# Optimization experiments

Hardware: AMD Instinct MI355X
Metric: run time of the kernel (lower is better)

## Reference

```python
import jax, jax.numpy as jnp
import numpy as np

B, S, D, H = 2, 2048, 2048, 16
DH = D // H  # 128


def _rope(x, cos, sin):
    # Faithful to the source: x is (B, H, S, Dh) (already transposed), and the
    # original apply_rotary_emb slices freqs_cis[:, :H, :] and broadcasts over
    # the S axis -> rotation angle depends on head index (source quirk).
    h = x.shape[1]
    c = cos[:, :h, :][:, :, None, :]  # (1, H, 1, Dh/2)
    s = sin[:, :h, :][:, :, None, :]
    half = x.shape[-1] // 2
    re, im = x[..., :half], x[..., half:]
    return jnp.concatenate([re * c - im * s, re * s + im * c], axis=-1)


def setup_inputs() -> dict:
    key = jax.random.key(0)
    k0, k1, k2 = jax.random.split(key, 3)
    x = jax.random.normal(k0, (B, S, D), jnp.float32)
    Wqkv = jax.random.normal(k1, (D, 3 * D), jnp.float32) / np.float32(np.sqrt(D))
    bqkv = jnp.zeros((3 * D,), jnp.float32)
    Wout = jax.random.normal(k2, (D, D), jnp.float32) / np.float32(np.sqrt(D))
    bout = jnp.zeros((D,), jnp.float32)
    # standard RoPE frequency table, stored as cos/sin (unit-modulus complex)
    inv_freq = 1.0 / (10000.0 ** (np.arange(0, DH // 2, dtype=np.float32) / (DH // 2)))
    ang = np.outer(np.arange(S, dtype=np.float32), inv_freq)  # (S, Dh/2)
    freqs_cos = jnp.asarray(np.cos(ang)[None], jnp.float32)   # (1, S, Dh/2)
    freqs_sin = jnp.asarray(np.sin(ang)[None], jnp.float32)
    mask = jnp.triu(jnp.ones((S, S), bool), 1)[None, None]    # causal, True = masked
    return {"x": x, "Wqkv": Wqkv, "bqkv": bqkv, "Wout": Wout, "bout": bout,
            "freqs_cos": freqs_cos, "freqs_sin": freqs_sin, "mask": mask}


def reference(x, Wqkv, bqkv, Wout, bout, freqs_cos, freqs_sin, mask):
    b, s, d = x.shape
    scale = DH ** (-0.5)
    qkv = x @ Wqkv + bqkv                                   # (B, S, 3D)
    q, k, v = jnp.split(qkv, 3, axis=-1)
    to_heads = lambda t: t.reshape(b, s, H, DH).transpose(0, 2, 1, 3)  # (B,H,S,Dh)
    q, k, v = to_heads(q), to_heads(k), to_heads(v)
    q = _rope(q, freqs_cos, freqs_sin)
    k = _rope(k, freqs_cos, freqs_sin)
    scores = jnp.einsum('bhqd,bhkd->bhqk', q, k) * scale
    scores = jnp.where(mask, -jnp.inf, scores)
    p = jax.nn.softmax(scores, axis=-1)                     # dropout p=0 (eval)
    out = jnp.einsum('bhqk,bhkd->bhqd', p, v)
    out = out.transpose(0, 2, 1, 3).reshape(b, s, d)
    return out @ Wout + bout
```

## Files before the change

kernel.cpp:

```cpp
#include <hip/hip_runtime.h>

#define S_ 2048
#define D_ 2048
#define H_ 16
#define DH_ 128

typedef __attribute__((ext_vector_type(8))) short short8;
typedef __attribute__((ext_vector_type(4))) float f32x4;
typedef __attribute__((ext_vector_type(8))) unsigned short ushort8;
typedef __attribute__((ext_vector_type(4))) unsigned short ushort4v;

__device__ __forceinline__ unsigned short f2bf(float f) {
  unsigned int u;
  __builtin_memcpy(&u, &f, 4);
  unsigned int lsb = (u >> 16) & 1u;
  u += 0x7fffu + lsb;
  return (unsigned short)(u >> 16);
}

__device__ __forceinline__ void gload_lds16(const void* g, void* l) {
  __builtin_amdgcn_global_load_lds(
      (const __attribute__((address_space(1))) unsigned int*)g,
      (__attribute__((address_space(3))) unsigned int*)l, 16, 0, 0);
}

template <int N> __device__ __forceinline__ void vmwait() {
  if constexpr (N == 8)      asm volatile("s_waitcnt vmcnt(8)" ::: "memory");
  else if constexpr (N == 6) asm volatile("s_waitcnt vmcnt(6)" ::: "memory");
  else if constexpr (N == 4) asm volatile("s_waitcnt vmcnt(4)" ::: "memory");
  else if constexpr (N == 3) asm volatile("s_waitcnt vmcnt(3)" ::: "memory");
  else if constexpr (N == 2) asm volatile("s_waitcnt vmcnt(2)" ::: "memory");
  else                       asm volatile("s_waitcnt vmcnt(0)" ::: "memory");
}

#define FENCE_ asm volatile("" ::: "memory")
#define BAR_ { FENCE_; __builtin_amdgcn_s_barrier(); FENCE_; }

__global__ void k_convert_x(const float* __restrict__ x, unsigned short* __restrict__ xb) {
  int idx = blockIdx.x * 256 + threadIdx.x;
  const float4* xv = (const float4*)x;
  float4 a = xv[(size_t)idx * 2];
  float4 b = xv[(size_t)idx * 2 + 1];
  ushort8 o;
  o[0] = f2bf(a.x); o[1] = f2bf(a.y); o[2] = f2bf(a.z); o[3] = f2bf(a.w);
  o[4] = f2bf(b.x); o[5] = f2bf(b.y); o[6] = f2bf(b.z); o[7] = f2bf(b.w);
  *(ushort8*)(xb + (size_t)idx * 8) = o;
}

__global__ void k_prep_w(const float* __restrict__ W, const float* __restrict__ cosb,
                         const float* __restrict__ sinb, unsigned short* __restrict__ WT,
                         int Nw, int rot_limit) {
  __shared__ float tile[32][129];
  const int t = threadIdx.x;
  const int kt = blockIdx.x * 32, nt = blockIdx.y * 128;
#pragma unroll
  for (int i = 0; i < 4; ++i) {
    int q = i * 256 + t;
    int kl = q >> 5, cq = q & 31;
    float4 v = *(const float4*)(W + (size_t)(kt + kl) * Nw + nt + cq * 4);
    tile[kl][cq * 4 + 0] = v.x; tile[kl][cq * 4 + 1] = v.y;
    tile[kl][cq * 4 + 2] = v.z; tile[kl][cq * 4 + 3] = v.w;
  }
  __syncthreads();
  const bool rot = nt < rot_limit;
#pragma unroll
  for (int i = 0; i < 16; ++i) {
    int f = i * 256 + t;
    int kl = f & 31, nl = f >> 5;
    int ng = nt + nl;
    float val;
    if (rot) {
      int i0 = nl & 63;
      int h = (ng & 2047) >> 7;
      float c = cosb[h * 64 + i0], sn = sinb[h * 64 + i0];
      float re = tile[kl][i0], im = tile[kl][i0 + 64];
      val = (nl < 64) ? (re * c - im * sn) : (re * sn + im * c);
    } else {
      val = tile[kl][nl];
    }
    WT[(size_t)ng * 2048 + kt + kl] = f2bf(val);
  }
}

template <int NF, int MODE>
__global__ __launch_bounds__(512, 2) void k_ms(
    const unsigned short* __restrict__ A, const unsigned short* __restrict__ Bt,
    const float* __restrict__ bias,
    unsigned short* __restrict__ Qb, unsigned short* __restrict__ Kb,
    unsigned short* __restrict__ Vt, float* __restrict__ Co) {
  constexpr int BN = NF * 64;
  constexpr int NT = 32;
  constexpr int BBASE = 65536;
  constexpr int BSZ = BN * 128;
  __shared__ unsigned char lds[BBASE + 3 * BSZ];

  const int tid = threadIdx.x, l = tid & 63, w = tid >> 6;
  const int wm = w >> 2, wn = w & 3;
  const int nwg = gridDim.x;
  const int bid = blockIdx.x;
  const int swz = (bid & 7) * (nwg >> 3) + (bid >> 3);
  const int tm = (swz & 15) * 256;
  const int tn = (swz >> 4) * BN;

  const int sslot = (l & 7) ^ (l >> 3);
  const unsigned short* aB = A + (size_t)(tm + (l >> 3)) * 2048 + sslot * 8;
  const unsigned short* bB = Bt + (size_t)(tn + (l >> 3)) * 2048 + sslot * 8;
  const int xg = ((l >> 4) ^ (l & 7)) << 4;
  const int afo = (wm * 128 + (l & 15)) * 128 + xg;
  const int bfo = (wn * (NF * 16) + (l & 15)) * 128 + xg;

  f32x4 acc[8][NF] = {};
  short8 af[8], bf[2 * NF];

#define SAF_(ab_, u_) {                                                         \
  _Pragma("unroll") for (int i_ = 0; i_ < 4; ++i_) {                            \
    int c_ = w + i_ * 8;                                                        \
    gload_lds16(aB + (size_t)(c_ * 8) * 2048 + (u_) * 64,                       \
                lds + (ab_) + c_ * 1024); } }
#define SBF_(bs_, u_) {                                                         \
  _Pragma("unroll") for (int i_ = 0; i_ < NF; ++i_) {                           \
    int c_ = w + i_ * 8;                                                        \
    gload_lds16(bB + (size_t)(c_ * 8) * 2048 + (u_) * 64,                       \
                lds + (bs_) + c_ * 1024); } }
#define RDA2_(ab_, mh_) {                                                       \
  _Pragma("unroll") for (int m_ = 0; m_ < 4; ++m_) {                            \
    unsigned a_ = (ab_) + afo + ((mh_) * 4 + m_) * 2048;                        \
    af[m_]     = *(const short8*)(lds + a_);                                    \
    af[4 + m_] = *(const short8*)(lds + (a_ ^ 64)); } }
#define RDB2_(bb_) {                                                            \
  _Pragma("unroll") for (int n_ = 0; n_ < NF; ++n_) {                           \
    unsigned a_ = (bb_) + bfo + n_ * 2048;                                      \
    bf[n_]      = *(const short8*)(lds + a_);                                   \
    bf[NF + n_] = *(const short8*)(lds + (a_ ^ 64)); } }
#define MMF_(mh_) { __builtin_amdgcn_s_setprio(1);                              \
  _Pragma("unroll") for (int kk_ = 0; kk_ < 2; ++kk_)                           \
  _Pragma("unroll") for (int m_ = 0; m_ < 4; ++m_)                              \
  _Pragma("unroll") for (int n_ = 0; n_ < NF; ++n_)                             \
    acc[(mh_) * 4 + m_][n_] = __builtin_amdgcn_mfma_f32_16x16x32_bf16(          \
        af[kk_ * 4 + m_], bf[kk_ * NF + n_], acc[(mh_) * 4 + m_][n_], 0, 0, 0); \
  __builtin_amdgcn_s_setprio(0); }

  SAF_(0u, 0); SBF_(BBASE, 0); SBF_(BBASE + BSZ, 1);
  vmwait<NF>(); BAR_;

  int bcur = 0, bstg = 2;
#pragma unroll 1
  for (int v = 0; v < NT; ++v) {
    const unsigned ab = (unsigned)(v & 1) * 32768u;
    const unsigned an = (unsigned)((v + 1) & 1) * 32768u;
    const unsigned bb = BBASE + (unsigned)bcur * BSZ;
    const unsigned bs = BBASE + (unsigned)bstg * BSZ;
    RDB2_(bb);
    RDA2_(ab, 0);
    if (v + 1 < NT) SAF_(an, v + 1);
    MMF_(0);
    RDA2_(ab, 1);
    if (v + 2 < NT) SBF_(bs, v + 2);
    MMF_(1);
    if (v < NT - 2) { vmwait<NF>(); } else { vmwait<0>(); }
    BAR_;
    bcur = (bcur == 2) ? 0 : bcur + 1;
    bstg = (bstg == 2) ? 0 : bstg + 1;
  }
#undef SAF_
#undef SBF_
#undef RDA2_
#undef RDB2_
#undef MMF_

  const int ln = l & 15, rb4 = (l >> 4) << 2;
#pragma unroll
  for (int m = 0; m < 8; ++m) {
    int rbase = tm + wm * 128 + m * 16 + rb4;
#pragma unroll
    for (int n = 0; n < NF; ++n) {
      int colg = tn + wn * (NF * 16) + n * 16 + ln;
      float bv = bias[colg];
      if constexpr (MODE == 0) {
        int reg = colg >> 11;
        int h = (colg & 2047) >> 7, dh = colg & 127;
        if (reg == 2) {
          int b = rbase >> 11, s = rbase & 2047;
          ushort4v o;
#pragma unroll
          for (int j = 0; j < 4; ++j) o[j] = f2bf(acc[m][n][j] + bv);
          *(ushort4v*)(Vt + ((size_t)(b * H_ + h) * DH_ + dh) * S_ + s) = o;
        } else {
#pragma unroll
          for (int j = 0; j < 4; ++j) {
            int r = rbase + j;
            int b = r >> 11, s = r & 2047;
            size_t off = ((size_t)(b * H_ + h) * S_ + s) * DH_ + dh;
            float v = acc[m][n][j] + bv;
            if (reg == 0) Qb[off] = f2bf(v * 0.08838834764831845f);
            else Kb[off] = f2bf(v);
          }
        }
      } else {
#pragma unroll
        for (int j = 0; j < 4; ++j)
          Co[(size_t)(rbase + j) * 2048 + colg] = acc[m][n][j] + bv;
      }
    }
  }
}

__global__ __launch_bounds__(512) void k_attn(
    const unsigned short* __restrict__ Qb, const unsigned short* __restrict__ Kb,
    const unsigned short* __restrict__ Vt, unsigned short* __restrict__ Ob) {
  __shared__ unsigned short kls[2][8192];
  __shared__ unsigned short vls[2][8192];
  __shared__ unsigned short pls[8192];
  const int t = threadIdx.x, l = t & 63, w = t >> 6;
  const int id = blockIdx.x;
  const int pairi = id >> 5, bh = id & 31;
  const int b = bh >> 4, h = bh & 15;
  const int lq = l & 15, lg = l >> 4;
  const int rb = lg << 2;
  const unsigned short* Qp = Qb + (size_t)bh * S_ * DH_;
  const unsigned short* Kp = Kb + (size_t)bh * S_ * DH_;
  const unsigned short* Vp = Vt + (size_t)bh * DH_ * S_;

#pragma unroll 1
  for (int half = 0; half < 2; ++half) {
    const int qt = half ? (15 - pairi) : pairi;
    const int qb = qt * 128;
    const int qrow = qb + w * 16 + lq;
    const int nkv = 2 * qt + 2;

    short8 qf[4];
#pragma unroll
    for (int c = 0; c < 4; ++c)
      qf[c] = *(const short8*)(Qp + (size_t)qrow * 128 + c * 32 + lg * 8);

    f32x4 o[8] = {};
    float m = -1e30f, lsum = 0.f;

#pragma unroll
    for (int i = 0; i < 2; ++i) {
      int cid = w + i * 8;
      int krow = cid * 4 + (l >> 4);
      int kslot = (l & 15) ^ (krow & 7);
      gload_lds16(Kp + (size_t)krow * 128 + kslot * 8, &kls[0][cid * 512]);
      int vrow = cid * 8 + (l >> 3);
      int vslot = (l & 7) ^ (vrow & 7);
      gload_lds16(Vp + (size_t)vrow * S_ + vslot * 8, &vls[0][cid * 512]);
    }
    __syncthreads();

#pragma unroll 1
    for (int kvt = 0; kvt < nkv; ++kvt) {
      const int kvb = kvt * 64;
      const int cur = kvt & 1;

      if (kvt + 1 < nkv) {
        const int kvb2 = kvb + 64;
#pragma unroll
        for (int i = 0; i < 2; ++i) {
          int cid = w + i * 8;
          int krow = cid * 4 + (l >> 4);
          int kslot = (l & 15) ^ (krow & 7);
          gload_lds16(Kp + (size_t)(kvb2 + krow) * 128 + kslot * 8,
                      &kls[cur ^ 1][cid * 512]);
          int vrow = cid * 8 + (l >> 3);
          int vslot = (l & 7) ^ (vrow & 7);
          gload_lds16(Vp + (size_t)vrow * S_ + kvb2 + vslot * 8,
                      &vls[cur ^ 1][cid * 512]);
        }
      }

      f32x4 sc[4];
      __builtin_amdgcn_s_setprio(1);
#pragma unroll
      for (int nb = 0; nb < 4; ++nb) {
        f32x4 sacc = {};
#pragma unroll
        for (int c = 0; c < 4; ++c) {
          int row = nb * 16 + lq;
          int off = (c * 64 + (lg * 16)) ^ ((row & 7) << 4);
          short8 kf = *(const short8*)((const char*)kls[cur] + row * 256 + off);
          sacc = __builtin_amdgcn_mfma_f32_16x16x32_bf16(kf, qf[c], sacc, 0, 0, 0);
        }
        sc[nb] = sacc;
      }
      __builtin_amdgcn_s_setprio(0);

      float xs[4][4];
      float xm = -1e30f;
      const bool diag = (kvb + 63) > (qb + w * 16);
#pragma unroll
      for (int nb = 0; nb < 4; ++nb)
#pragma unroll
        for (int r = 0; r < 4; ++r) {
          float x = sc[nb][r];
          if (diag && (kvb + nb * 16 + rb + r > qrow)) x = -1e30f;
          xs[nb][r] = x;
          xm = fmaxf(xm, x);
        }
      xm = fmaxf(xm, __shfl_xor(xm, 16));
      xm = fmaxf(xm, __shfl_xor(xm, 32));

      if (__any(xm > m + 8.f)) {
        float nm = fmaxf(m, xm);
        float f = __expf(m - nm);
        m = nm; lsum *= f;
        float fj[4];
#pragma unroll
        for (int j = 0; j < 4; ++j) fj[j] = __shfl(f, (l & 48) | (rb + j));
#pragma unroll
        for (int d = 0; d < 8; ++d) {
          o[d][0] *= fj[0]; o[d][1] *= fj[1]; o[d][2] *= fj[2]; o[d][3] *= fj[3];
        }
      }
      float s = 0.f;
#pragma unroll
      for (int nb = 0; nb < 4; ++nb)
#pragma unroll
        for (int r = 0; r < 4; ++r) {
          float p = __expf(xs[nb][r] - m);
          xs[nb][r] = p;
          s += p;
        }
      s += __shfl_xor(s, 16);
      s += __shfl_xor(s, 32);
      lsum += s;

#pragma unroll
      for (int nb = 0; nb < 4; ++nb) {
        ushort4v pw;
#pragma unroll
        for (int r = 0; r < 4; ++r) pw[r] = f2bf(xs[nb][r]);
        *(ushort4v*)((char*)pls + w * 2048 + lq * 128 +
                     ((nb * 32 + lg * 8) ^ ((lq & 7) << 4))) = pw;
      }

      __builtin_amdgcn_s_setprio(1);
#pragma unroll
      for (int kc = 0; kc < 2; ++kc) {
        short8 pa = *(const short8*)((const char*)pls + w * 2048 + lq * 128 +
                                     ((kc * 64 + lg * 16) ^ ((lq & 7) << 4)));
#pragma unroll
        for (int d = 0; d < 8; ++d) {
          int vrow = d * 16 + lq;
          int voff = (kc * 64 + (lg * 16)) ^ ((vrow & 7) << 4);
          short8 vf = *(const short8*)((const char*)vls[cur] + vrow * 128 + voff);
          o[d] = __builtin_amdgcn_mfma_f32_16x16x32_bf16(pa, vf, o[d], 0, 0, 0);
        }
      }
      __builtin_amdgcn_s_setprio(0);
      __syncthreads();
    }

    float inv = 1.f / lsum;
    float invj[4];
#pragma unroll
    for (int j = 0; j < 4; ++j) invj[j] = __shfl(inv, (l & 48) | (rb + j));
#pragma unroll
    for (int d = 0; d < 8; ++d) {
#pragma unroll
      for (int j = 0; j < 4; ++j) {
        int s = qb + w * 16 + rb + j;
        int col = h * 128 + d * 16 + lq;
        Ob[((size_t)(b * S_ + s)) * D_ + col] = f2bf(o[d][j] * invj[j]);
      }
    }
  }
}

extern "C" void kernel_launch(void* const* d_in, const int* in_sizes, int n_in,
                              void* d_out, int out_size, void* d_ws, size_t ws_size,
                              hipStream_t stream) {
  const float* x    = (const float*)d_in[0];
  const float* Wqkv = (const float*)d_in[1];
  const float* bqkv = (const float*)d_in[2];
  const float* Wout = (const float*)d_in[3];
  const float* bout = (const float*)d_in[4];
  const float* fcos = (const float*)d_in[5];
  const float* fsin = (const float*)d_in[6];
  float* out = (float*)d_out;

  char* ws = (char*)d_ws;
  unsigned short* xbf   = (unsigned short*)(ws);
  unsigned short* wqkvT = (unsigned short*)(ws + 16777216);
  unsigned short* woutT = (unsigned short*)(ws + 41943040);
  unsigned short* Qb    = (unsigned short*)(ws + 50331648);
  unsigned short* Kb    = Qb + 8388608;
  unsigned short* Vtb   = Kb + 8388608;
  unsigned short* Ob    = xbf;

  hipLaunchKernelGGL(k_convert_x, dim3(4096), dim3(256), 0, stream, x, xbf);
  hipLaunchKernelGGL(k_prep_w, dim3(64, 48), dim3(256), 0, stream,
                     Wqkv, fcos, fsin, wqkvT, 6144, 4096);
  hipLaunchKernelGGL(k_prep_w, dim3(64, 16), dim3(256), 0, stream,
                     Wout, fcos, fsin, woutT, 2048, 0);
  hipLaunchKernelGGL((k_ms<3, 0>), dim3(512), dim3(512), 0, stream,
                     xbf, wqkvT, bqkv, Qb, Kb, Vtb, (float*)nullptr);
  hipLaunchKernelGGL(k_attn, dim3(256), dim3(512), 0, stream, Qb, Kb, Vtb, Ob);
  hipLaunchKernelGGL((k_ms<2, 1>), dim3(256), dim3(512), 0, stream,
                     Ob, woutT, bout, (unsigned short*)nullptr,
                     (unsigned short*)nullptr, (unsigned short*)nullptr, out);
}
```

Baseline: 251.9 us.

## Merge input/weight prep kernels into one launch and remap GEMM tile order

Combines the x-to-bf16 conversion and both weight transpose/RoPE-prep kernels into a single kernel dispatched by block index, cutting two launches and the gaps between them. It also replaces the GEMM workgroup-to-tile swizzle with an explicit mapping that interleaves M and N tiles across the low bits of the block id, presumably to spread neighbouring workgroups across XCDs for better L2 reuse. The new mapping hard-codes grid sizes, so it only works for these exact launch dimensions.

New measurement: 238.4 us, median of 2. -5.4%, faster.

```diff
diff --git a/kernel.cpp b/kernel.cpp
--- a/kernel.cpp
+++ b/kernel.cpp
@@ -36,23 +36,11 @@
 #define FENCE_ asm volatile("" ::: "memory")
 #define BAR_ { FENCE_; __builtin_amdgcn_s_barrier(); FENCE_; }
 
-__global__ void k_convert_x(const float* __restrict__ x, unsigned short* __restrict__ xb) {
-  int idx = blockIdx.x * 256 + threadIdx.x;
-  const float4* xv = (const float4*)x;
-  float4 a = xv[(size_t)idx * 2];
-  float4 b = xv[(size_t)idx * 2 + 1];
-  ushort8 o;
-  o[0] = f2bf(a.x); o[1] = f2bf(a.y); o[2] = f2bf(a.z); o[3] = f2bf(a.w);
-  o[4] = f2bf(b.x); o[5] = f2bf(b.y); o[6] = f2bf(b.z); o[7] = f2bf(b.w);
-  *(ushort8*)(xb + (size_t)idx * 8) = o;
-}
-
-__global__ void k_prep_w(const float* __restrict__ W, const float* __restrict__ cosb,
-                         const float* __restrict__ sinb, unsigned short* __restrict__ WT,
-                         int Nw, int rot_limit) {
-  __shared__ float tile[32][129];
+__device__ __forceinline__ void prep_w_tile(
+    const float* __restrict__ W, const float* __restrict__ cosb,
+    const float* __restrict__ sinb, unsigned short* __restrict__ WT,
+    int Nw, int rot_limit, int kt, int nt, float (*tile)[129]) {
   const int t = threadIdx.x;
-  const int kt = blockIdx.x * 32, nt = blockIdx.y * 128;
 #pragma unroll
   for (int i = 0; i < 4; ++i) {
     int q = i * 256 + t;
@@ -82,6 +70,32 @@
   }
 }
 
+__global__ void k_prep(const float* __restrict__ x, unsigned short* __restrict__ xb,
+                       const float* __restrict__ Wqkv, const float* __restrict__ Wout,
+                       const float* __restrict__ cosb, const float* __restrict__ sinb,
+                       unsigned short* __restrict__ wqkvT, unsigned short* __restrict__ woutT) {
+  __shared__ float tile[32][129];
+  const int bid = blockIdx.x;
+  if (bid < 4096) {
+    int idx = bid * 256 + threadIdx.x;
+    const float4* xv = (const float4*)x;
+    float4 a = xv[(size_t)idx * 2];
+    float4 b = xv[(size_t)idx * 2 + 1];
+    ushort8 o;
+    o[0] = f2bf(a.x); o[1] = f2bf(a.y); o[2] = f2bf(a.z); o[3] = f2bf(a.w);
+    o[4] = f2bf(b.x); o[5] = f2bf(b.y); o[6] = f2bf(b.z); o[7] = f2bf(b.w);
+    *(ushort8*)(xb + (size_t)idx * 8) = o;
+  } else if (bid < 7168) {
+    int b2 = bid - 4096;
+    prep_w_tile(Wqkv, cosb, sinb, wqkvT, 6144, 4096,
+                (b2 & 63) * 32, (b2 >> 6) * 128, tile);
+  } else {
+    int b3 = bid - 7168;
+    prep_w_tile(Wout, cosb, sinb, woutT, 2048, 0,
+                (b3 & 63) * 32, (b3 >> 6) * 128, tile);
+  }
+}
+
 template <int NF, int MODE>
 __global__ __launch_bounds__(512, 2) void k_ms(
     const unsigned short* __restrict__ A, const unsigned short* __restrict__ Bt,
@@ -96,11 +110,13 @@
 
   const int tid = threadIdx.x, l = tid & 63, w = tid >> 6;
   const int wm = w >> 2, wn = w & 3;
-  const int nwg = gridDim.x;
   const int bid = blockIdx.x;
-  const int swz = (bid & 7) * (nwg >> 3) + (bid >> 3);
-  const int tm = (swz & 15) * 256;
-  const int tn = (swz >> 4) * BN;
+  int tmi = (bid & 1) * 8 + ((bid >> 3) & 7);
+  int tni;
+  if constexpr (NF == 3) tni = ((bid >> 1) & 3) * 8 + (bid >> 6);
+  else                   tni = ((bid >> 1) & 3) * 4 + (bid >> 6);
+  const int tm = tmi * 256;
+  const int tn = tni * BN;
 
   const int sslot = (l & 7) ^ (l >> 3);
   const unsigned short* aB = A + (size_t)(tm + (l >> 3)) * 2048 + sslot * 8;
@@ -388,11 +404,8 @@
   unsigned short* Vtb   = Kb + 8388608;
   unsigned short* Ob    = xbf;
 
-  hipLaunchKernelGGL(k_convert_x, dim3(4096), dim3(256), 0, stream, x, xbf);
-  hipLaunchKernelGGL(k_prep_w, dim3(64, 48), dim3(256), 0, stream,
-                     Wqkv, fcos, fsin, wqkvT, 6144, 4096);
-  hipLaunchKernelGGL(k_prep_w, dim3(64, 16), dim3(256), 0, stream,
-                     Wout, fcos, fsin, woutT, 2048, 0);
+  hipLaunchKernelGGL(k_prep, dim3(8192), dim3(256), 0, stream,
+                     x, xbf, Wqkv, Wout, fcos, fsin, wqkvT, woutT);
   hipLaunchKernelGGL((k_ms<3, 0>), dim3(512), dim3(512), 0, stream,
                      xbf, wqkvT, bqkv, Qb, Kb, Vtb, (float*)nullptr);
   hipLaunchKernelGGL(k_attn, dim3(256), dim3(512), 0, stream, Qb, Kb, Vtb, Ob);
```
